# Kernel tuning notes

Measured on AMD Instinct MI355X. Metric: run time of the kernel, lower is better.

Reference implementation:

```python
import jax, jax.numpy as jnp
import numpy as np

GCN_DIMS = [128, 16, 32, 64]  # input_dim, then hardcoded hidden dims
OUT_DIM = 10
N_NODES = 8192


def setup_inputs() -> dict:
    key = jax.random.key(0)
    ks = jax.random.split(key, 12)
    x = jax.random.normal(ks[0], (N_NODES, GCN_DIMS[0]), dtype=jnp.float32)
    adj = jax.random.uniform(ks[1], (N_NODES, N_NODES), dtype=jnp.float32)
    # row-normalize so aggregation is well-scaled (like a normalized adjacency)
    adj = adj / jnp.sum(adj, axis=1, keepdims=True)
    inp = {"x": x, "adj": adj}
    # GCN layer weights (nn.Linear: y = x @ W.T + b; we store W as [in, out])
    for i in range(3):
        din, dout = GCN_DIMS[i], GCN_DIMS[i + 1]
        s = 1.0 / np.sqrt(din)
        inp[f"W{i}"] = jax.random.uniform(ks[2 + 2 * i], (din, dout), minval=-s, maxval=s, dtype=jnp.float32)
        inp[f"b{i}"] = jax.random.uniform(ks[3 + 2 * i], (dout,), minval=-s, maxval=s, dtype=jnp.float32)
    # output head: Linear(64,32) -> ReLU -> Linear(32,10)
    s = 1.0 / np.sqrt(64)
    inp["Wo0"] = jax.random.uniform(ks[8], (64, 32), minval=-s, maxval=s, dtype=jnp.float32)
    inp["bo0"] = jax.random.uniform(ks[9], (32,), minval=-s, maxval=s, dtype=jnp.float32)
    s = 1.0 / np.sqrt(32)
    inp["Wo1"] = jax.random.uniform(ks[10], (32, OUT_DIM), minval=-s, maxval=s, dtype=jnp.float32)
    inp["bo1"] = jax.random.uniform(ks[11], (OUT_DIM,), minval=-s, maxval=s, dtype=jnp.float32)
    return inp


def reference(x, adj, W0, b0, W1, b1, W2, b2, Wo0, bo0, Wo1, bo1):
    # Three GCN layers: linear transform -> adjacency aggregation -> ReLU
    # (dropout treated as identity: inference-mode reference)
    for W, b in ((W0, b0), (W1, b1), (W2, b2)):
        h = x @ W + b              # [N, dout]
        h = adj @ h                # [N, dout] graph aggregation
        x = jax.nn.relu(h)
    # output head
    x = jax.nn.relu(x @ Wo0 + bo0)
    return x @ Wo1 + bo1           # [N, OUT_DIM]
```

## Files before the change

### kernel.cpp

```cpp
#include <hip/hip_runtime.h>

#define N 8192

typedef __attribute__((ext_vector_type(8))) short short8;
typedef __attribute__((ext_vector_type(4))) float f32x4;
typedef __attribute__((ext_vector_type(2))) float f32x2;

#define ADJ_SC 4096.0f
#define ADJ_ISC (1.0f / 4096.0f)

__device__ __forceinline__ unsigned short f2bf(float f) {
    union { float f; unsigned int u; } v; v.f = f;
    unsigned int r = v.u + 0x7FFFu + ((v.u >> 16) & 1u);
    return (unsigned short)(r >> 16);
}

__device__ __forceinline__ void gl2lds16(const void* g, void* l) {
    __builtin_amdgcn_global_load_lds(
        (const __attribute__((address_space(1))) unsigned int*)g,
        (__attribute__((address_space(3))) unsigned int*)l, 16, 0, 0);
}

__device__ __forceinline__ short8 fp8x8_to_bf16x8(uint2 a8) {
    short8 r;
    #pragma unroll
    for (int d = 0; d < 2; ++d) {
        unsigned int src = (d == 0) ? a8.x : a8.y;
        f32x2 lo = __builtin_amdgcn_cvt_pk_f32_fp8(src, false);
        f32x2 hi = __builtin_amdgcn_cvt_pk_f32_fp8(src, true);
        r[4 * d + 0] = (short)(__builtin_bit_cast(unsigned int, lo[0]) >> 16);
        r[4 * d + 1] = (short)(__builtin_bit_cast(unsigned int, lo[1]) >> 16);
        r[4 * d + 2] = (short)(__builtin_bit_cast(unsigned int, hi[0]) >> 16);
        r[4 * d + 3] = (short)(__builtin_bit_cast(unsigned int, hi[1]) >> 16);
    }
    return r;
}

#define BAR_SCHED() do { __builtin_amdgcn_s_barrier(); \
                         __builtin_amdgcn_sched_barrier(0); } while (0)

template<int NC, int BK, int MODE>
__global__ __launch_bounds__(256) void agg_kernel(
    const float* __restrict__ adj,
    const unsigned char* __restrict__ adj_b_in,
    unsigned char* __restrict__ adj_b_out,
    const unsigned short* __restrict__ hT,
    float* __restrict__ y,
    int klen)
{
    constexpr int BM = 64;
    constexpr int NCT = NC / 16;

    const int tid = threadIdx.x;
    const int w  = tid >> 6;
    const int l  = tid & 63;
    const int hi = l >> 4;
    const int lr = l & 15;
    const int row0 = blockIdx.x * BM;
    const int k00  = blockIdx.y * klen;
    const int nt   = klen / BK;

    f32x4 acc[NCT];
    #pragma unroll
    for (int i = 0; i < NCT; ++i) acc[i] = f32x4{0.f, 0.f, 0.f, 0.f};

    if constexpr (MODE == 2) {
        __shared__ unsigned char as2_[2][BM * BK];
        __shared__ unsigned short hs2_[2][NC * BK];
        constexpr int TA = (BM * BK) / 1024;
        constexpr int TH = (NC * 2 * BK) / 1024;
        constexpr int GRA = BK / 16, RPA = 1024 / BK;
        constexpr int GRH = (2 * BK) / 16, RPH = 1024 / (2 * BK);
        constexpr int KW = (TA + TH) / 4;

        auto stage = [&](char* ab, char* hb, int t) {
            const int kb = k00 + t * BK;
            #pragma unroll
            for (int i = w; i < TA; i += 4) {
                int r = i * RPA + l / GRA, g = l % GRA;
                gl2lds16(adj_b_in + (size_t)(row0 + r) * N + kb + 16 * g,
                         ab + i * 1024);
            }
            #pragma unroll
            for (int i = w; i < TH; i += 4) {
                int c = i * RPH + l / GRH, g = l % GRH;
                gl2lds16(hT + (size_t)c * N + kb + 8 * g, hb + i * 1024);
            }
        };

        stage((char*)as2_[0], (char*)hs2_[0], 0);
        for (int t = 0; t < nt; ++t) {
            char* ca = (char*)as2_[t & 1];
            char* ch = (char*)hs2_[t & 1];
            char* na = (char*)as2_[(t & 1) ^ 1];
            char* nh = (char*)hs2_[(t & 1) ^ 1];
            if (t + 1 < nt) {
                stage(na, nh, t + 1);
                asm volatile("s_waitcnt vmcnt(%0)" :: "n"(KW) : "memory");
            } else {
                asm volatile("s_waitcnt vmcnt(0)" ::: "memory");
            }
            BAR_SCHED();
            #pragma unroll
            for (int kk = 0; kk < BK; kk += 32) {
                const int arow = 16 * w + lr;
                uint2 a8 = *reinterpret_cast<const uint2*>(
                    ca + arow * BK + ((kk + 8 * hi) ^ ((arow & 7) << 3)));
                short8 a = fp8x8_to_bf16x8(a8);
                #pragma unroll
                for (int ct = 0; ct < NCT; ++ct) {
                    const int bcol = 16 * ct + lr;
                    short8 b = *reinterpret_cast<const short8*>(
                        ch + bcol * (2 * BK) + ((2 * kk + 16 * hi) ^ ((bcol & 7) << 4)));
                    acc[ct] = __builtin_amdgcn_mfma_f32_16x16x32_bf16(a, b, acc[ct], 0, 0, 0);
                }
            }
            asm volatile("s_waitcnt lgkmcnt(0)" ::: "memory");
            BAR_SCHED();
        }
        #pragma unroll
        for (int ct = 0; ct < NCT; ++ct)
            #pragma unroll
            for (int r = 0; r < 4; ++r) acc[ct][r] *= ADJ_ISC;
    } else {
        __shared__ unsigned short as_[BM * BK];
        __shared__ unsigned short hs_[NC * BK];
        char* asb = (char*)as_;
        char* hsb = (char*)hs_;
        constexpr int ROWB = BK * 2;
        constexpr int LV = 8;
        constexpr int TH = (NC * ROWB) / 1024;
        float4 pf[LV];
        #pragma unroll
        for (int it = 0; it < LV; ++it) {
            int idx = tid + it * 256, r = idx >> 5, q = idx & 31;
            const f32x4* p = reinterpret_cast<const f32x4*>(
                adj + (size_t)(row0 + r) * N + k00 + 4 * q);
            f32x4 t0 = __builtin_nontemporal_load(p);
            pf[it] = float4{t0[0], t0[1], t0[2], t0[3]};
        }
        for (int t = 0; t < nt; ++t) {
            const int kb = k00 + t * BK;
            #pragma unroll
            for (int i = w; i < TH; i += 4) {
                int c = i * 4 + l / 16;
                int g = l % 16;
                gl2lds16(hT + (size_t)c * N + kb + 8 * g, hsb + i * 1024);
            }
            __builtin_amdgcn_sched_barrier(0);
            #pragma unroll
            for (int it = 0; it < LV; ++it) {
                int idx = tid + it * 256, r = idx >> 5, q = idx & 31;
                ushort4 u;
                u.x = f2bf(pf[it].x); u.y = f2bf(pf[it].y);
                u.z = f2bf(pf[it].z); u.w = f2bf(pf[it].w);
                if (MODE == 1) {
                    unsigned int pk = 0;
                    pk = __builtin_amdgcn_cvt_pk_fp8_f32(
                        pf[it].x * ADJ_SC, pf[it].y * ADJ_SC, pk, false);
                    pk = __builtin_amdgcn_cvt_pk_fp8_f32(
                        pf[it].z * ADJ_SC, pf[it].w * ADJ_SC, pk, true);
                    *reinterpret_cast<unsigned int*>(
                        adj_b_out + (size_t)(row0 + r) * N + kb +
                        ((4 * q) ^ ((r & 7) << 3))) = pk;
                }
                *reinterpret_cast<ushort4*>(
                    asb + r * ROWB + ((8 * q) ^ ((r & 7) << 4))) = u;
            }
            __builtin_amdgcn_sched_barrier(0);
            if (t + 1 < nt) {
                #pragma unroll
                for (int it = 0; it < LV; ++it) {
                    int idx = tid + it * 256, r = idx >> 5, q = idx & 31;
                    const f32x4* p = reinterpret_cast<const f32x4*>(
                        adj + (size_t)(row0 + r) * N + kb + BK + 4 * q);
                    f32x4 t0 = __builtin_nontemporal_load(p);
                    pf[it] = float4{t0[0], t0[1], t0[2], t0[3]};
                }
                __builtin_amdgcn_sched_barrier(0);
                if (MODE == 1)
                    asm volatile("s_waitcnt vmcnt(16) lgkmcnt(0)" ::: "memory");
                else
                    asm volatile("s_waitcnt vmcnt(8) lgkmcnt(0)" ::: "memory");
            } else {
                if (MODE == 1)
                    asm volatile("s_waitcnt vmcnt(8) lgkmcnt(0)" ::: "memory");
                else
                    asm volatile("s_waitcnt vmcnt(0) lgkmcnt(0)" ::: "memory");
            }
            BAR_SCHED();
            #pragma unroll
            for (int kk = 0; kk < BK; kk += 32) {
                const int arow = 16 * w + lr;
                short8 a = *reinterpret_cast<const short8*>(
                    asb + arow * ROWB + ((2 * kk + 16 * hi) ^ ((arow & 7) << 4)));
                #pragma unroll
                for (int ct = 0; ct < NCT; ++ct) {
                    const int bcol = 16 * ct + lr;
                    short8 b = *reinterpret_cast<const short8*>(
                        hsb + bcol * ROWB + ((2 * kk + 16 * hi) ^ ((bcol & 7) << 4)));
                    acc[ct] = __builtin_amdgcn_mfma_f32_16x16x32_bf16(a, b, acc[ct], 0, 0, 0);
                }
            }
            asm volatile("s_waitcnt lgkmcnt(0)" ::: "memory");
            BAR_SCHED();
        }
    }
    float* yp = y + (size_t)blockIdx.y * N * NC;
    #pragma unroll
    for (int ct = 0; ct < NCT; ++ct) {
        #pragma unroll
        for (int r = 0; r < 4; ++r) {
            yp[(size_t)(row0 + 16 * w + 4 * hi + r) * NC + 16 * ct + lr] = acc[ct][r];
        }
    }
}

__global__ __launch_bounds__(256) void lin0_kernel(
    const float* __restrict__ x, const float* __restrict__ W,
    const float* __restrict__ b, unsigned short* __restrict__ hT)
{
    __shared__ float xs[64][129];
    const int tid = threadIdx.x;
    const int row0 = blockIdx.x * 64;
    #pragma unroll
    for (int it = 0; it < 8; ++it) {
        int idx = tid + it * 256;
        int r = idx >> 5, q = idx & 31;
        float4 v = *reinterpret_cast<const float4*>(x + (size_t)(row0 + r) * 128 + 4 * q);
        xs[r][4 * q + 0] = v.x; xs[r][4 * q + 1] = v.y;
        xs[r][4 * q + 2] = v.z; xs[r][4 * q + 3] = v.w;
    }
    __syncthreads();
    const int w = tid >> 6, l = tid & 63;
    float acc[4] = {b[w], b[w + 4], b[w + 8], b[w + 12]};
    for (int k = 0; k < 128; ++k) {
        float xv = xs[l][k];
        #pragma unroll
        for (int cc = 0; cc < 4; ++cc) acc[cc] += xv * W[k * 16 + w + 4 * cc];
    }
    #pragma unroll
    for (int cc = 0; cc < 4; ++cc) {
        int c = w + 4 * cc;
        hT[(size_t)c * N + ((row0 + l) ^ ((c & 7) << 3))] = f2bf(acc[cc]);
    }
}

template<int NIN, int NOUT, int S>
__global__ __launch_bounds__(256) void mid_linear_kernel(
    const float* __restrict__ y,
    const float* __restrict__ W,
    const float* __restrict__ b,
    unsigned short* __restrict__ hT)
{
    __shared__ float xs[64][NIN + 1];
    const int tid = threadIdx.x;
    const int row0 = blockIdx.x * 64;
    constexpr int NF4 = 64 * NIN / 4;
    #pragma unroll
    for (int idx0 = 0; idx0 < NF4; idx0 += 256) {
        int idx = idx0 + tid;
        if (NF4 >= 256 || idx < NF4) {
            int r = idx / (NIN / 4), q = idx % (NIN / 4);
            size_t off = (size_t)(row0 + r) * NIN + 4 * q;
            float4 v = *reinterpret_cast<const float4*>(y + off);
            #pragma unroll
            for (int s = 1; s < S; ++s) {
                float4 t = *reinterpret_cast<const float4*>(y + (size_t)s * N * NIN + off);
                v.x += t.x; v.y += t.y; v.z += t.z; v.w += t.w;
            }
            xs[r][4 * q + 0] = fmaxf(v.x, 0.f);
            xs[r][4 * q + 1] = fmaxf(v.y, 0.f);
            xs[r][4 * q + 2] = fmaxf(v.z, 0.f);
            xs[r][4 * q + 3] = fmaxf(v.w, 0.f);
        }
    }
    __syncthreads();
    const int w = tid >> 6, l = tid & 63;
    constexpr int CC = NOUT / 4;
    float acc[CC];
    #pragma unroll
    for (int cc = 0; cc < CC; ++cc) acc[cc] = b[w + 4 * cc];
    for (int k = 0; k < NIN; ++k) {
        float xv = xs[l][k];
        #pragma unroll
        for (int cc = 0; cc < CC; ++cc) acc[cc] += xv * W[k * NOUT + w + 4 * cc];
    }
    #pragma unroll
    for (int cc = 0; cc < CC; ++cc) {
        int c = w + 4 * cc;
        hT[(size_t)c * N + ((row0 + l) ^ ((c & 7) << 3))] = f2bf(acc[cc]);
    }
}

template<int S>
__global__ __launch_bounds__(256) void head_kernel(
    const float* __restrict__ y,
    const float* __restrict__ Wo0, const float* __restrict__ bo0,
    const float* __restrict__ Wo1, const float* __restrict__ bo1,
    float* __restrict__ out)
{
    __shared__ float xr[16][68];
    __shared__ float hid[16][36];
    const int tid = threadIdx.x;
    const int row0 = blockIdx.x * 16;
    {
        int r = tid >> 4, q = tid & 15;
        float4 v = *reinterpret_cast<const float4*>(
            y + ((size_t)(row0 + r)) * 64 + 4 * q);
        #pragma unroll
        for (int s = 1; s < S; ++s) {
            float4 t = *reinterpret_cast<const float4*>(
                y + ((size_t)s * N + row0 + r) * 64 + 4 * q);
            v.x += t.x; v.y += t.y; v.z += t.z; v.w += t.w;
        }
        xr[r][4 * q + 0] = fmaxf(v.x, 0.f);
        xr[r][4 * q + 1] = fmaxf(v.y, 0.f);
        xr[r][4 * q + 2] = fmaxf(v.z, 0.f);
        xr[r][4 * q + 3] = fmaxf(v.w, 0.f);
    }
    __syncthreads();
    {
        int j = tid & 31, r0 = tid >> 5;
        #pragma unroll
        for (int rr = r0; rr < 16; rr += 8) {
            float a = bo0[j];
            #pragma unroll
            for (int k = 0; k < 64; ++k) a += xr[rr][k] * Wo0[k * 32 + j];
            hid[rr][j] = fmaxf(a, 0.f);
        }
    }
    __syncthreads();
    if (tid < 160) {
        int r = tid / 10, c = tid % 10;
        float a = bo1[c];
        #pragma unroll
        for (int k = 0; k < 32; ++k) a += hid[r][k] * Wo1[k * 10 + c];
        out[(size_t)(row0 + r) * 10 + c] = a;
    }
}

extern "C" void kernel_launch(void* const* d_in, const int* in_sizes, int n_in,
                              void* d_out, int out_size, void* d_ws, size_t ws_size,
                              hipStream_t stream) {
    const float* x   = (const float*)d_in[0];
    const float* adj = (const float*)d_in[1];
    const float* W0  = (const float*)d_in[2];
    const float* b0  = (const float*)d_in[3];
    const float* W1  = (const float*)d_in[4];
    const float* b1  = (const float*)d_in[5];
    const float* W2  = (const float*)d_in[6];
    const float* b2  = (const float*)d_in[7];
    const float* Wo0 = (const float*)d_in[8];
    const float* bo0 = (const float*)d_in[9];
    const float* Wo1 = (const float*)d_in[10];
    const float* bo1 = (const float*)d_in[11];
    float* out = (float*)d_out;

    char* ws = (char*)d_ws;
    constexpr int S = 16;
    constexpr int KLEN = N / S;
    float* y_part          = (float*)ws;
    unsigned short* hT     = (unsigned short*)(ws + (32u << 20));
    unsigned char* adj_b   = (unsigned char*)(ws + (34u << 20));
    const size_t NEED_FULL = ((size_t)34 << 20) + (size_t)N * N;
    const bool cache = ws_size >= NEED_FULL;

    lin0_kernel<<<128, 256, 0, stream>>>(x, W0, b0, hT);

    if (cache)
        agg_kernel<16, 128, 1><<<dim3(128, S), 256, 0, stream>>>(adj, nullptr, adj_b, hT, y_part, KLEN);
    else
        agg_kernel<16, 128, 0><<<dim3(128, S), 256, 0, stream>>>(adj, nullptr, nullptr, hT, y_part, KLEN);

    mid_linear_kernel<16, 32, S><<<128, 256, 0, stream>>>(y_part, W1, b1, hT);

    if (cache)
        agg_kernel<32, 64, 2><<<dim3(128, S), 256, 0, stream>>>(nullptr, adj_b, nullptr, hT, y_part, KLEN);
    else
        agg_kernel<32, 128, 0><<<dim3(128, S), 256, 0, stream>>>(adj, nullptr, nullptr, hT, y_part, KLEN);

    mid_linear_kernel<32, 64, S><<<128, 256, 0, stream>>>(y_part, W2, b2, hT);

    if (cache)
        agg_kernel<64, 64, 2><<<dim3(128, S), 256, 0, stream>>>(nullptr, adj_b, nullptr, hT, y_part, KLEN);
    else
        agg_kernel<64, 128, 0><<<dim3(128, S), 256, 0, stream>>>(adj, nullptr, nullptr, hT, y_part, KLEN);

    head_kernel<S><<<512, 256, 0, stream>>>(y_part, Wo0, bo0, Wo1, bo1, out);
}
```

Measured before the change: 138.8 us.

## Store split-K partials in bf16, shrink tile K, halve split count for later layers

```diff
diff --git a/kernel.cpp b/kernel.cpp
--- a/kernel.cpp
+++ b/kernel.cpp
@@ -13,6 +13,10 @@
     union { float f; unsigned int u; } v; v.f = f;
     unsigned int r = v.u + 0x7FFFu + ((v.u >> 16) & 1u);
     return (unsigned short)(r >> 16);
+}
+
+__device__ __forceinline__ float bf2f(unsigned short u) {
+    return __builtin_bit_cast(float, (unsigned int)u << 16);
 }
 
 __device__ __forceinline__ void gl2lds16(const void* g, void* l) {
@@ -45,7 +49,7 @@
     const unsigned char* __restrict__ adj_b_in,
     unsigned char* __restrict__ adj_b_out,
     const unsigned short* __restrict__ hT,
-    float* __restrict__ y,
+    unsigned short* __restrict__ y,
     int klen)
 {
     constexpr int BM = 64;
@@ -128,12 +132,15 @@
         char* asb = (char*)as_;
         char* hsb = (char*)hs_;
         constexpr int ROWB = BK * 2;
-        constexpr int LV = 8;
+        constexpr int LV = (BM * BK) / (4 * 256);
+        constexpr int GQ = BK / 4;
         constexpr int TH = (NC * ROWB) / 1024;
+        constexpr int RPH = 1024 / ROWB;
+        constexpr int GRH = ROWB / 16;
         float4 pf[LV];
         #pragma unroll
         for (int it = 0; it < LV; ++it) {
-            int idx = tid + it * 256, r = idx >> 5, q = idx & 31;
+            int idx = tid + it * 256, r = idx / GQ, q = idx % GQ;
             const f32x4* p = reinterpret_cast<const f32x4*>(
                 adj + (size_t)(row0 + r) * N + k00 + 4 * q);
             f32x4 t0 = __builtin_nontemporal_load(p);
@@ -143,14 +150,13 @@
             const int kb = k00 + t * BK;
             #pragma unroll
             for (int i = w; i < TH; i += 4) {
-                int c = i * 4 + l / 16;
-                int g = l % 16;
+                int c = i * RPH + l / GRH, g = l % GRH;
                 gl2lds16(hT + (size_t)c * N + kb + 8 * g, hsb + i * 1024);
             }
             __builtin_amdgcn_sched_barrier(0);
             #pragma unroll
             for (int it = 0; it < LV; ++it) {
-                int idx = tid + it * 256, r = idx >> 5, q = idx & 31;
+                int idx = tid + it * 256, r = idx / GQ, q = idx % GQ;
                 ushort4 u;
                 u.x = f2bf(pf[it].x); u.y = f2bf(pf[it].y);
                 u.z = f2bf(pf[it].z); u.w = f2bf(pf[it].w);
@@ -171,7 +177,7 @@
             if (t + 1 < nt) {
                 #pragma unroll
                 for (int it = 0; it < LV; ++it) {
-                    int idx = tid + it * 256, r = idx >> 5, q = idx & 31;
+                    int idx = tid + it * 256, r = idx / GQ, q = idx % GQ;
                     const f32x4* p = reinterpret_cast<const f32x4*>(
                         adj + (size_t)(row0 + r) * N + kb + BK + 4 * q);
                     f32x4 t0 = __builtin_nontemporal_load(p);
@@ -179,12 +185,12 @@
                 }
                 __builtin_amdgcn_sched_barrier(0);
                 if (MODE == 1)
-                    asm volatile("s_waitcnt vmcnt(16) lgkmcnt(0)" ::: "memory");
+                    asm volatile("s_waitcnt vmcnt(8) lgkmcnt(0)" ::: "memory");
                 else
-                    asm volatile("s_waitcnt vmcnt(8) lgkmcnt(0)" ::: "memory");
+                    asm volatile("s_waitcnt vmcnt(4) lgkmcnt(0)" ::: "memory");
             } else {
                 if (MODE == 1)
-                    asm volatile("s_waitcnt vmcnt(8) lgkmcnt(0)" ::: "memory");
+                    asm volatile("s_waitcnt vmcnt(4) lgkmcnt(0)" ::: "memory");
                 else
                     asm volatile("s_waitcnt vmcnt(0) lgkmcnt(0)" ::: "memory");
             }
@@ -206,12 +212,13 @@
             BAR_SCHED();
         }
     }
-    float* yp = y + (size_t)blockIdx.y * N * NC;
+    unsigned short* yp = y + (size_t)blockIdx.y * N * NC;
     #pragma unroll
     for (int ct = 0; ct < NCT; ++ct) {
         #pragma unroll
         for (int r = 0; r < 4; ++r) {
-            yp[(size_t)(row0 + 16 * w + 4 * hi + r) * NC + 16 * ct + lr] = acc[ct][r];
+            yp[(size_t)(row0 + 16 * w + 4 * hi + r) * NC + 16 * ct + lr] =
+                f2bf(acc[ct][r]);
         }
     }
 }
@@ -248,7 +255,7 @@
 
 template<int NIN, int NOUT, int S>
 __global__ __launch_bounds__(256) void mid_linear_kernel(
-    const float* __restrict__ y,
+    const unsigned short* __restrict__ y,
     const float* __restrict__ W,
     const float* __restrict__ b,
     unsigned short* __restrict__ hT)
@@ -263,16 +270,18 @@
         if (NF4 >= 256 || idx < NF4) {
             int r = idx / (NIN / 4), q = idx % (NIN / 4);
             size_t off = (size_t)(row0 + r) * NIN + 4 * q;
-            float4 v = *reinterpret_cast<const float4*>(y + off);
-            #pragma unroll
-            for (int s = 1; s < S; ++s) {
-                float4 t = *reinterpret_cast<const float4*>(y + (size_t)s * N * NIN + off);
-                v.x += t.x; v.y += t.y; v.z += t.z; v.w += t.w;
-            }
-            xs[r][4 * q + 0] = fmaxf(v.x, 0.f);
-            xs[r][4 * q + 1] = fmaxf(v.y, 0.f);
-            xs[r][4 * q + 2] = fmaxf(v.z, 0.f);
-            xs[r][4 * q + 3] = fmaxf(v.w, 0.f);
+            float s0 = 0.f, s1 = 0.f, s2 = 0.f, s3 = 0.f;
+            #pragma unroll
+            for (int s = 0; s < S; ++s) {
+                ushort4 t = *reinterpret_cast<const ushort4*>(
+                    y + (size_t)s * N * NIN + off);
+                s0 += bf2f(t.x); s1 += bf2f(t.y);
+                s2 += bf2f(t.z); s3 += bf2f(t.w);
+            }
+            xs[r][4 * q + 0] = fmaxf(s0, 0.f);
+            xs[r][4 * q + 1] = fmaxf(s1, 0.f);
+            xs[r][4 * q + 2] = fmaxf(s2, 0.f);
+            xs[r][4 * q + 3] = fmaxf(s3, 0.f);
         }
     }
     __syncthreads();
@@ -295,7 +304,7 @@
 
 template<int S>
 __global__ __launch_bounds__(256) void head_kernel(
-    const float* __restrict__ y,
+    const unsigned short* __restrict__ y,
     const float* __restrict__ Wo0, const float* __restrict__ bo0,
     const float* __restrict__ Wo1, const float* __restrict__ bo1,
     float* __restrict__ out)
@@ -306,18 +315,19 @@
     const int row0 = blockIdx.x * 16;
     {
         int r = tid >> 4, q = tid & 15;
-        float4 v = *reinterpret_cast<const float4*>(
-            y + ((size_t)(row0 + r)) * 64 + 4 * q);
-        #pragma unroll
-        for (int s = 1; s < S; ++s) {
-            float4 t = *reinterpret_cast<const float4*>(
-                y + ((size_t)s * N + row0 + r) * 64 + 4 * q);
-            v.x += t.x; v.y += t.y; v.z += t.z; v.w += t.w;
-        }
-        xr[r][4 * q + 0] = fmaxf(v.x, 0.f);
-        xr[r][4 * q + 1] = fmaxf(v.y, 0.f);
-        xr[r][4 * q + 2] = fmaxf(v.z, 0.f);
-        xr[r][4 * q + 3] = fmaxf(v.w, 0.f);
+        size_t off = (size_t)(row0 + r) * 64 + 4 * q;
+        float s0 = 0.f, s1 = 0.f, s2 = 0.f, s3 = 0.f;
+        #pragma unroll
+        for (int s = 0; s < S; ++s) {
+            ushort4 t = *reinterpret_cast<const ushort4*>(
+                y + (size_t)s * N * 64 + off);
+            s0 += bf2f(t.x); s1 += bf2f(t.y);
+            s2 += bf2f(t.z); s3 += bf2f(t.w);
+        }
+        xr[r][4 * q + 0] = fmaxf(s0, 0.f);
+        xr[r][4 * q + 1] = fmaxf(s1, 0.f);
+        xr[r][4 * q + 2] = fmaxf(s2, 0.f);
+        xr[r][4 * q + 3] = fmaxf(s3, 0.f);
     }
     __syncthreads();
     {
@@ -358,34 +368,34 @@
     float* out = (float*)d_out;
 
     char* ws = (char*)d_ws;
-    constexpr int S = 16;
-    constexpr int KLEN = N / S;
-    float* y_part          = (float*)ws;
-    unsigned short* hT     = (unsigned short*)(ws + (32u << 20));
-    unsigned char* adj_b   = (unsigned char*)(ws + (34u << 20));
-    const size_t NEED_FULL = ((size_t)34 << 20) + (size_t)N * N;
+    constexpr int S1 = 16;
+    constexpr int S2 = 8;
+    unsigned short* y_part = (unsigned short*)ws;
+    unsigned short* hT     = (unsigned short*)(ws + (16u << 20));
+    unsigned char* adj_b   = (unsigned char*)(ws + (18u << 20));
+    const size_t NEED_FULL = ((size_t)18 << 20) + (size_t)N * N;
     const bool cache = ws_size >= NEED_FULL;
 
     lin0_kernel<<<128, 256, 0, stream>>>(x, W0, b0, hT);
 
     if (cache)
-        agg_kernel<16, 128, 1><<<dim3(128, S), 256, 0, stream>>>(adj, nullptr, adj_b, hT, y_part, KLEN);
+        agg_kernel<16, 64, 1><<<dim3(128, S1), 256, 0, stream>>>(adj, nullptr, adj_b, hT, y_part, N / S1);
     else
-        agg_kernel<16, 128, 0><<<dim3(128, S), 256, 0, stream>>>(adj, nullptr, nullptr, hT, y_part, KLEN);
-
-    mid_linear_kernel<16, 32, S><<<128, 256, 0, stream>>>(y_part, W1, b1, hT);
+        agg_kernel<16, 64, 0><<<dim3(128, S1), 256, 0, stream>>>(adj, nullptr, nullptr, hT, y_part, N / S1);
+
+    mid_linear_kernel<16, 32, S1><<<128, 256, 0, stream>>>(y_part, W1, b1, hT);
 
     if (cache)
-        agg_kernel<32, 64, 2><<<dim3(128, S), 256, 0, stream>>>(nullptr, adj_b, nullptr, hT, y_part, KLEN);
+        agg_kernel<32, 64, 2><<<dim3(128, S2), 256, 0, stream>>>(nullptr, adj_b, nullptr, hT, y_part, N / S2);
     else
-        agg_kernel<32, 128, 0><<<dim3(128, S), 256, 0, stream>>>(adj, nullptr, nullptr, hT, y_part, KLEN);
-
-    mid_linear_kernel<32, 64, S><<<128, 256, 0, stream>>>(y_part, W2, b2, hT);
+        agg_kernel<32, 64, 0><<<dim3(128, S2), 256, 0, stream>>>(adj, nullptr, nullptr, hT, y_part, N / S2);
+
+    mid_linear_kernel<32, 64, S2><<<128, 256, 0, stream>>>(y_part, W2, b2, hT);
 
     if (cache)
-        agg_kernel<64, 64, 2><<<dim3(128, S), 256, 0, stream>>>(nullptr, adj_b, nullptr, hT, y_part, KLEN);
+        agg_kernel<64, 64, 2><<<dim3(128, S2), 256, 0, stream>>>(nullptr, adj_b, nullptr, hT, y_part, N / S2);
     else
-        agg_kernel<64, 128, 0><<<dim3(128, S), 256, 0, stream>>>(adj, nullptr, nullptr, hT, y_part, KLEN);
-
-    head_kernel<S><<<512, 256, 0, stream>>>(y_part, Wo0, bo0, Wo1, bo1, out);
-}
+        agg_kernel<64, 64, 0><<<dim3(128, S2), 256, 0, stream>>>(adj, nullptr, nullptr, hT, y_part, N / S2);
+
+    head_kernel<S2><<<512, 256, 0, stream>>>(y_part, Wo0, bo0, Wo1, bo1, out);
+}
```

Result: slower. 142.5 us (+2.7%).
